# Kernel tuning notes

Hardware: AMD Instinct MI355X
Metric: run time of the kernel (lower is better)

## Reference

```python
import jax, jax.numpy as jnp
import numpy as np

B, T, C = 4, 2048, 1024
H = 16
D = C // H  # head_size = 64


def setup_inputs() -> dict:
    key = jax.random.key(0)
    ks = jax.random.split(key, 6)
    s = 0.02
    x = jax.random.normal(ks[0], (B, T, C), dtype=jnp.float32)
    # per-head projections (bias=False), stacked over heads: [H, C, D]
    Wq = jax.random.normal(ks[1], (H, C, D), dtype=jnp.float32) * s
    Wk = jax.random.normal(ks[2], (H, C, D), dtype=jnp.float32) * s
    Wv = jax.random.normal(ks[3], (H, C, D), dtype=jnp.float32) * s
    # output projection Linear(H*D, C)
    Wo = jax.random.normal(ks[4], (H * D, C), dtype=jnp.float32) * s
    bo = jax.random.normal(ks[5], (C,), dtype=jnp.float32) * s
    return {"x": x, "Wq": Wq, "Wk": Wk, "Wv": Wv, "Wo": Wo, "bo": bo}


def reference(x, Wq, Wk, Wv, Wo, bo):
    # q,k,v: [B, H, T, D]
    q = jnp.einsum('btc,hcd->bhtd', x, Wq)
    k = jnp.einsum('btc,hcd->bhtd', x, Wk)
    v = jnp.einsum('btc,hcd->bhtd', x, Wv)
    scale = 1.0 / jnp.sqrt(jnp.asarray(D, dtype=x.dtype))
    scores = jnp.einsum('bhtd,bhsd->bhts', q, k) * scale  # [B,H,T,T]
    causal = jnp.tril(jnp.ones((T, T), dtype=bool))
    scores = jnp.where(causal, scores, jnp.asarray(-jnp.inf, dtype=scores.dtype))
    wei = jax.nn.softmax(scores, axis=-1)
    out = jnp.einsum('bhts,bhsd->bhtd', wei, v)  # [B,H,T,D]
    # concat heads along last dim (head order = module list order)
    out = jnp.transpose(out, (0, 2, 1, 3)).reshape(B, T, H * D)
    return out @ Wo + bo
```

## Files before the change

### kernel.cpp

```cpp
#include <hip/hip_runtime.h>
#include <math.h>

typedef __attribute__((ext_vector_type(8))) short short8;
typedef __attribute__((ext_vector_type(4))) short short4v;
typedef __attribute__((ext_vector_type(4))) float floatx4;

#define AS1 __attribute__((address_space(1)))
#define AS3 __attribute__((address_space(3)))

__device__ inline void gload_lds16(const short* g, short* l) {
    __builtin_amdgcn_global_load_lds((const AS1 unsigned int*)g,
                                     (AS3 unsigned int*)l, 16, 0, 0);
}

__device__ inline short f2bf(float f) {
    unsigned u = __builtin_bit_cast(unsigned, f);
    u += 0x7fffu + ((u >> 16) & 1u);
    return (short)(u >> 16);
}

__global__ __launch_bounds__(256) void conv_x(
    const float* __restrict__ x, short* __restrict__ xb)
{
    int i = (blockIdx.x * 256 + threadIdx.x) * 4;
    float4 v = *(const float4*)&x[i];
    short4v o = { f2bf(v.x), f2bf(v.y), f2bf(v.z), f2bf(v.w) };
    *(short4v*)&xb[i] = o;
}

__global__ __launch_bounds__(256) void transpose_w(
    const float* __restrict__ Wq, const float* __restrict__ Wk,
    const float* __restrict__ Wv, const float* __restrict__ Wo,
    short* __restrict__ Wall, short* __restrict__ WoT)
{
    __shared__ short T[64 * 72];
    const int kt = blockIdx.x, y = blockIdx.y;
    const int tid = threadIdx.x;
    const int lr = tid >> 2, lc = (tid & 3) * 16;
    #pragma unroll 1
    for (int m = 0; m < 4; ++m) {
        const float* src;
        float s = 1.f;
        if (m < 3) {
            const float* W = (m == 0) ? Wq : (m == 1) ? Wk : Wv;
            src = W + ((size_t)y << 16) + (size_t)(kt * 64 + lr) * 64 + lc;
            if (m == 0) s = 0.125f * 1.44269504088896f;
        } else {
            src = Wo + (size_t)(kt * 64 + lr) * 1024 + y * 64 + lc;
        }
        short8 t0, t1;
        {
            float4 v0 = *(const float4*)(src + 0);
            float4 v1 = *(const float4*)(src + 4);
            float4 v2 = *(const float4*)(src + 8);
            float4 v3 = *(const float4*)(src + 12);
            t0[0]=f2bf(v0.x*s); t0[1]=f2bf(v0.y*s); t0[2]=f2bf(v0.z*s); t0[3]=f2bf(v0.w*s);
            t0[4]=f2bf(v1.x*s); t0[5]=f2bf(v1.y*s); t0[6]=f2bf(v1.z*s); t0[7]=f2bf(v1.w*s);
            t1[0]=f2bf(v2.x*s); t1[1]=f2bf(v2.y*s); t1[2]=f2bf(v2.z*s); t1[3]=f2bf(v2.w*s);
            t1[4]=f2bf(v3.x*s); t1[5]=f2bf(v3.y*s); t1[6]=f2bf(v3.z*s); t1[7]=f2bf(v3.w*s);
        }
        *(short8*)&T[lr * 72 + lc]     = t0;
        *(short8*)&T[lr * 72 + lc + 8] = t1;
        __syncthreads();
        short8 o0, o1;
        #pragma unroll
        for (int j = 0; j < 8; ++j) o0[j] = T[(lc + j) * 72 + lr];
        #pragma unroll
        for (int j = 0; j < 8; ++j) o1[j] = T[(lc + 8 + j) * 72 + lr];
        short* dst = (m < 3)
            ? Wall + (size_t)(m * 1024 + y * 64 + lr) * 1024 + kt * 64
            : WoT  + (size_t)(y * 64 + lr) * 1024 + kt * 64;
        *(short8*)&dst[lc]     = o0;
        *(short8*)&dst[lc + 8] = o1;
        __syncthreads();
    }
}

__global__ __launch_bounds__(256) void gemm_bt(
    const short* __restrict__ A, const short* __restrict__ BT,
    short* __restrict__ C, short* __restrict__ Vt, int M, int N, int K)
{
    __shared__ short As[128 * 64];
    __shared__ short Bs[128 * 64];
    const int tid  = threadIdx.x;
    const int wid  = tid >> 6, lane = tid & 63;
    const int quad = lane >> 4, l15 = lane & 15;
    const int l7 = l15 & 7;
    const int m0 = blockIdx.x * 128, n0 = blockIdx.y * 128;
    const int wr = (wid >> 1) * 64, wc = (wid & 1) * 64;

    floatx4 acc[4][4] = {};

    const int srow = tid >> 3;
    const int gcol = ((tid & 7) ^ (srow & 7)) * 8;

    for (int k0 = 0; k0 < K; k0 += 64) {
        #pragma unroll
        for (int t = 0; t < 4; ++t) {
            gload_lds16(A  + (size_t)(m0 + srow + t * 32) * K + k0 + gcol,
                        &As[(t * 32 + wid * 8) * 64]);
            gload_lds16(BT + (size_t)(n0 + srow + t * 32) * K + k0 + gcol,
                        &Bs[(t * 32 + wid * 8) * 64]);
        }
        __syncthreads();
        #pragma unroll
        for (int ks = 0; ks < 2; ++ks) {
            short8 bfr[4];
            #pragma unroll
            for (int j = 0; j < 4; ++j)
                bfr[j] = *(const short8*)&Bs[(wc + j * 16 + l15) * 64 +
                                             (((ks * 4 + quad) ^ l7) * 8)];
            #pragma unroll
            for (int i = 0; i < 4; ++i) {
                short8 afr = *(const short8*)&As[(wr + i * 16 + l15) * 64 +
                                                 (((ks * 4 + quad) ^ l7) * 8)];
                #pragma unroll
                for (int j = 0; j < 4; ++j)
                    acc[i][j] = __builtin_amdgcn_mfma_f32_16x16x32_bf16(
                        afr, bfr[j], acc[i][j], 0, 0, 0);
            }
        }
        __syncthreads();
    }

    const int plane = n0 >> 10;
    #pragma unroll
    for (int i = 0; i < 4; ++i) {
        int row = m0 + wr + i * 16 + quad * 4;
        #pragma unroll
        for (int j = 0; j < 4; ++j) {
            int col = n0 + wc + j * 16 + l15;
            int c1 = col & 1023;
            if (plane < 2) {
                short* dst = C + (size_t)plane * 8192 * 1024;
                #pragma unroll
                for (int r = 0; r < 4; ++r)
                    dst[(size_t)(row + r) * 1024 + c1] = f2bf(acc[i][j][r]);
            } else {
                int b = row >> 11, t = row & 2047;
                int hb = b * 16 + (c1 >> 6), d = c1 & 63;
                short4v o = { f2bf(acc[i][j][0]), f2bf(acc[i][j][1]),
                              f2bf(acc[i][j][2]), f2bf(acc[i][j][3]) };
                *(short4v*)&Vt[((size_t)hb * 64 + d) * 2048 + t] = o;
            }
        }
    }
}

__global__ __launch_bounds__(256) void gemm_o(
    const short* __restrict__ A, const short* __restrict__ BT,
    float* __restrict__ Cf, const float* __restrict__ bias, int N, int K)
{
    __shared__ short As[64 * 64];
    __shared__ short Bs[128 * 64];
    const int tid  = threadIdx.x;
    const int wid  = tid >> 6, lane = tid & 63;
    const int quad = lane >> 4, l15 = lane & 15;
    const int l7 = l15 & 7;
    const int m0 = blockIdx.x * 64, n0 = blockIdx.y * 128;
    const int wr = (wid >> 1) * 32, wc = (wid & 1) * 64;

    floatx4 acc[2][4] = {};

    const int srow = tid >> 3;
    const int gcol = ((tid & 7) ^ (srow & 7)) * 8;

    for (int k0 = 0; k0 < K; k0 += 64) {
        #pragma unroll
        for (int t = 0; t < 2; ++t)
            gload_lds16(A + (size_t)(m0 + srow + t * 32) * K + k0 + gcol,
                        &As[(t * 32 + wid * 8) * 64]);
        #pragma unroll
        for (int t = 0; t < 4; ++t)
            gload_lds16(BT + (size_t)(n0 + srow + t * 32) * K + k0 + gcol,
                        &Bs[(t * 32 + wid * 8) * 64]);
        __syncthreads();
        #pragma unroll
        for (int ks = 0; ks < 2; ++ks) {
            short8 bfr[4];
            #pragma unroll
            for (int j = 0; j < 4; ++j)
                bfr[j] = *(const short8*)&Bs[(wc + j * 16 + l15) * 64 +
                                             (((ks * 4 + quad) ^ l7) * 8)];
            #pragma unroll
            for (int i = 0; i < 2; ++i) {
                short8 afr = *(const short8*)&As[(wr + i * 16 + l15) * 64 +
                                                 (((ks * 4 + quad) ^ l7) * 8)];
                #pragma unroll
                for (int j = 0; j < 4; ++j)
                    acc[i][j] = __builtin_amdgcn_mfma_f32_16x16x32_bf16(
                        afr, bfr[j], acc[i][j], 0, 0, 0);
            }
        }
        __syncthreads();
    }

    #pragma unroll
    for (int i = 0; i < 2; ++i) {
        int row = m0 + wr + i * 16 + quad * 4;
        #pragma unroll
        for (int j = 0; j < 4; ++j) {
            int col = n0 + wc + j * 16 + l15;
            float bv = bias[col];
            #pragma unroll
            for (int r = 0; r < 4; ++r)
                Cf[(size_t)(row + r) * N + col] = acc[i][j][r] + bv;
        }
    }
}

__global__ __launch_bounds__(256) void attn_fwd(
    const short* __restrict__ Q, const short* __restrict__ Kg,
    const short* __restrict__ Vt_g, short* __restrict__ O)
{
    __shared__ short Ks[2][64 * 64];
    __shared__ short Vs[2][64 * 64];
    __shared__ short Pb[4 * 32 * 72];
    const int tid  = threadIdx.x;
    const int wid  = tid >> 6, lane = tid & 63;
    const int quad = lane >> 4, l15 = lane & 15;

    const int flat = blockIdx.x;
    const int xr = flat & 7;
    const int qq = flat >> 3;
    const int qt = 15 - (qq >> 3);
    const int hb = xr * 8 + (qq & 7);
    const int h = hb & 15, b = hb >> 4;

    const size_t base  = ((size_t)b * 2048) * 1024 + h * 64;
    const size_t vbase = ((size_t)(b * 16 + h)) * 64 * 2048;
    short* Pw = &Pb[wid * 32 * 72];

    const int srow = tid >> 3;
    const int gcol = ((tid & 7) ^ (srow & 7)) * 8;
    const int lbase0 = (wid * 8) * 64;
    const int lbase1 = (wid * 8 + 32) * 64;
    const int l7 = l15 & 7;

    const short one_bf = (short)0x3F80;
    const short8 bones = { one_bf, one_bf, one_bf, one_bf,
                           one_bf, one_bf, one_bf, one_bf };

    short8 qf[2][2];
    #pragma unroll
    for (int mt = 0; mt < 2; ++mt)
        #pragma unroll
        for (int ks = 0; ks < 2; ++ks)
            qf[mt][ks] = *(const short8*)&Q[base +
                (size_t)(qt * 128 + wid * 32 + mt * 16 + l15) * 1024 + ks * 32 + quad * 8];

    floatx4 oacc[2][4] = {};
    floatx4 lacc[2] = {};
    const int dst = 2 * qt + (wid >> 1);
    const int nst = 2 * qt + 2;

    const short* kptr = Kg + base + (size_t)srow * 1024 + gcol;
    const short* vptr = Vt_g + vbase + (size_t)srow * 2048 + gcol;

    gload_lds16(kptr,               &Ks[0][lbase0]);
    gload_lds16(kptr + 32 * 1024,   &Ks[0][lbase1]);
    gload_lds16(vptr,               &Vs[0][lbase0]);
    gload_lds16(vptr + 32 * 2048,   &Vs[0][lbase1]);
    kptr += 64 * 1024; vptr += 64;
    __syncthreads();

    for (int st = 0; st < nst; ++st) {
        const short* K0 = Ks[st & 1];
        const short* V0 = Vs[st & 1];
        if (st + 1 < nst) {
            short* K1 = Ks[(st + 1) & 1];
            short* V1 = Vs[(st + 1) & 1];
            gload_lds16(kptr,             &K1[lbase0]);
            gload_lds16(kptr + 32 * 1024, &K1[lbase1]);
            gload_lds16(vptr,             &V1[lbase0]);
            gload_lds16(vptr + 32 * 2048, &V1[lbase1]);
            kptr += 64 * 1024; vptr += 64;
        }

        if (st <= dst) {
            floatx4 sf[2][4];
            #pragma unroll
            for (int nt = 0; nt < 4; ++nt) {
                floatx4 z0 = {}, z1 = {};
                #pragma unroll
                for (int ks = 0; ks < 2; ++ks) {
                    short8 bfr = *(const short8*)&K0[(nt * 16 + l15) * 64 +
                                                     (((ks * 4 + quad) ^ l7) * 8)];
                    z0 = __builtin_amdgcn_mfma_f32_16x16x32_bf16(qf[0][ks], bfr, z0, 0, 0, 0);
                    z1 = __builtin_amdgcn_mfma_f32_16x16x32_bf16(qf[1][ks], bfr, z1, 0, 0, 0);
                }
                sf[0][nt] = z0; sf[1][nt] = z1;
            }

            if (st == dst) {
                #pragma unroll
                for (int mt = 0; mt < 2; ++mt)
                    #pragma unroll
                    for (int nt = 0; nt < 4; ++nt)
                        #pragma unroll
                        for (int r = 0; r < 4; ++r) {
                            int qa = qt * 128 + wid * 32 + mt * 16 + quad * 4 + r;
                            int sa = st * 64 + nt * 16 + l15;
                            if (sa > qa) sf[mt][nt][r] = -INFINITY;
                        }
            }

            #pragma unroll
            for (int mt = 0; mt < 2; ++mt)
                #pragma unroll
                for (int nt = 0; nt < 4; ++nt)
                    #pragma unroll
                    for (int r = 0; r < 4; ++r) {
                        float p = __builtin_amdgcn_exp2f(sf[mt][nt][r]);
                        unsigned u = __builtin_bit_cast(unsigned, p);
                        Pw[(mt * 16 + quad * 4 + r) * 72 + ((nt ^ quad) * 16) + l15] =
                            (short)(u >> 16);
                    }

            #pragma unroll
            for (int ks = 0; ks < 2; ++ks) {
                int blk = (ks * 2 + (quad >> 1)) ^ (l15 >> 2);
                short8 af0 = *(const short8*)&Pw[(l15) * 72 + blk * 16 + (quad & 1) * 8];
                short8 af1 = *(const short8*)&Pw[(16 + l15) * 72 + blk * 16 + (quad & 1) * 8];
                lacc[0] = __builtin_amdgcn_mfma_f32_16x16x32_bf16(af0, bones, lacc[0], 0, 0, 0);
                lacc[1] = __builtin_amdgcn_mfma_f32_16x16x32_bf16(af1, bones, lacc[1], 0, 0, 0);
                #pragma unroll
                for (int nt = 0; nt < 4; ++nt) {
                    short8 bfr = *(const short8*)&V0[(nt * 16 + l15) * 64 +
                                                     (((ks * 4 + quad) ^ l7) * 8)];
                    oacc[0][nt] = __builtin_amdgcn_mfma_f32_16x16x32_bf16(af0, bfr, oacc[0][nt], 0, 0, 0);
                    oacc[1][nt] = __builtin_amdgcn_mfma_f32_16x16x32_bf16(af1, bfr, oacc[1][nt], 0, 0, 0);
                }
            }
        }
        __syncthreads();
    }

    #pragma unroll
    for (int mt = 0; mt < 2; ++mt)
        #pragma unroll
        for (int nt = 0; nt < 4; ++nt)
            #pragma unroll
            for (int r = 0; r < 4; ++r) {
                float v = oacc[mt][nt][r] / lacc[mt][r];
                int qa = qt * 128 + wid * 32 + mt * 16 + quad * 4 + r;
                O[base + (size_t)qa * 1024 + nt * 16 + l15] = f2bf(v);
            }
}

extern "C" void kernel_launch(void* const* d_in, const int* in_sizes, int n_in,
                              void* d_out, int out_size, void* d_ws, size_t ws_size,
                              hipStream_t stream) {
    const float* x  = (const float*)d_in[0];
    const float* Wq = (const float*)d_in[1];
    const float* Wk = (const float*)d_in[2];
    const float* Wv = (const float*)d_in[3];
    const float* Wo = (const float*)d_in[4];
    const float* bo = (const float*)d_in[5];
    float* out = (float*)d_out;

    char* ws = (char*)d_ws;
    const size_t MB = 1024 * 1024;
    short* xb   = (short*)(ws + 0 * MB);
    short* Ao   = (short*)(ws + 0 * MB);
    short* Vt_g = (short*)(ws + 16 * MB);
    short* Wall = (short*)(ws + 32 * MB);
    short* WoT  = (short*)(ws + 38 * MB);
    short* Qp   = (short*)d_out;
    short* Kp   = Qp + 8 * 1024 * 1024;

    conv_x<<<8192, 256, 0, stream>>>(x, xb);
    transpose_w<<<dim3(16, 16), 256, 0, stream>>>(Wq, Wk, Wv, Wo, Wall, WoT);

    gemm_bt<<<dim3(64, 24), 256, 0, stream>>>(xb, Wall, Qp, Vt_g, 8192, 3072, 1024);

    attn_fwd<<<1024, 256, 0, stream>>>(Qp, Kp, Vt_g, Ao);

    gemm_o<<<dim3(128, 8), 256, 0, stream>>>(Ao, WoT, out, bo, 1024, 1024);
}
```

Measured before the change: 254.7 us.

## Double-buffer LDS tiles in projection GEMM to overlap loads with MFMA

The projection GEMM now keeps two LDS buffers for the A and B tiles and issues the global-to-LDS loads for the next k-tile before computing on the current one. This drops one barrier per iteration and lets memory latency hide behind MFMA work. All A fragments are also loaded into registers before the MFMA loop. In exchange, LDS use per block doubles to 64KB, which may reduce occupancy, and register pressure rises.

```diff
diff --git a/kernel.cpp b/kernel.cpp
--- a/kernel.cpp
+++ b/kernel.cpp
@@ -80,12 +80,11 @@
     const short* __restrict__ A, const short* __restrict__ BT,
     short* __restrict__ C, short* __restrict__ Vt, int M, int N, int K)
 {
-    __shared__ short As[128 * 64];
-    __shared__ short Bs[128 * 64];
+    __shared__ short As[2][128 * 64];
+    __shared__ short Bs[2][128 * 64];
     const int tid  = threadIdx.x;
     const int wid  = tid >> 6, lane = tid & 63;
-    const int quad = lane >> 4, l15 = lane & 15;
-    const int l7 = l15 & 7;
+    const int quad = lane >> 4, l15 = lane & 15, l7 = l15 & 7;
     const int m0 = blockIdx.x * 128, n0 = blockIdx.y * 128;
     const int wr = (wid >> 1) * 64, wc = (wid & 1) * 64;
 
@@ -93,35 +92,48 @@
 
     const int srow = tid >> 3;
     const int gcol = ((tid & 7) ^ (srow & 7)) * 8;
-
-    for (int k0 = 0; k0 < K; k0 += 64) {
-        #pragma unroll
-        for (int t = 0; t < 4; ++t) {
-            gload_lds16(A  + (size_t)(m0 + srow + t * 32) * K + k0 + gcol,
-                        &As[(t * 32 + wid * 8) * 64]);
-            gload_lds16(BT + (size_t)(n0 + srow + t * 32) * K + k0 + gcol,
-                        &Bs[(t * 32 + wid * 8) * 64]);
-        }
-        __syncthreads();
+    const int lrow = wid * 8;
+    const int NT = K >> 6;
+
+    const short* aCur = A  + (size_t)(m0 + srow) * K + gcol;
+    const short* bCur = BT + (size_t)(n0 + srow) * K + gcol;
+
+#define STAGE(c) do { \
+    _Pragma("unroll") \
+    for (int tt = 0; tt < 4; ++tt) { \
+        gload_lds16(aCur + (size_t)(tt * 32) * K, &As[c][(tt * 32 + lrow) * 64]); \
+        gload_lds16(bCur + (size_t)(tt * 32) * K, &Bs[c][(tt * 32 + lrow) * 64]); \
+    } \
+    aCur += 64; bCur += 64; } while (0)
+
+    STAGE(0);
+    __syncthreads();
+
+    for (int t = 0; t < NT; ++t) {
+        if (t + 1 < NT) STAGE((t + 1) & 1);
+        const short* Ab = As[t & 1];
+        const short* Bb = Bs[t & 1];
         #pragma unroll
         for (int ks = 0; ks < 2; ++ks) {
-            short8 bfr[4];
+            short8 bfr[4], afr[4];
             #pragma unroll
             for (int j = 0; j < 4; ++j)
-                bfr[j] = *(const short8*)&Bs[(wc + j * 16 + l15) * 64 +
+                bfr[j] = *(const short8*)&Bb[(wc + j * 16 + l15) * 64 +
                                              (((ks * 4 + quad) ^ l7) * 8)];
             #pragma unroll
-            for (int i = 0; i < 4; ++i) {
-                short8 afr = *(const short8*)&As[(wr + i * 16 + l15) * 64 +
-                                                 (((ks * 4 + quad) ^ l7) * 8)];
+            for (int i = 0; i < 4; ++i)
+                afr[i] = *(const short8*)&Ab[(wr + i * 16 + l15) * 64 +
+                                             (((ks * 4 + quad) ^ l7) * 8)];
+            #pragma unroll
+            for (int i = 0; i < 4; ++i)
                 #pragma unroll
                 for (int j = 0; j < 4; ++j)
                     acc[i][j] = __builtin_amdgcn_mfma_f32_16x16x32_bf16(
-                        afr, bfr[j], acc[i][j], 0, 0, 0);
-            }
-        }
-        __syncthreads();
-    }
+                        afr[i], bfr[j], acc[i][j], 0, 0, 0);
+        }
+        __syncthreads();
+    }
+#undef STAGE
 
     const int plane = n0 >> 10;
     #pragma unroll
```

Result: faster. 246.4 us (-3.3%).
